# Kernel optimization log

Hardware: AMD Instinct MI355X
Metric: run time of the kernel (lower is better)

Reference implementation:

```python
import jax, jax.numpy as jnp
import numpy as np

N_NODES = 100000
N_EDGES = 1600000
IN_F = 256
OUT_F = 128


def setup_inputs() -> dict:
    key = jax.random.key(0)
    k1, k2, k3, k4, k5, k6 = jax.random.split(key, 6)
    x = jax.random.normal(k1, (N_NODES, IN_F), dtype=jnp.float32)
    edge_row = jax.random.randint(k2, (N_EDGES,), 0, N_NODES, dtype=jnp.int32)
    edge_col = jax.random.randint(k3, (N_EDGES,), 0, N_NODES, dtype=jnp.int32)
    edge_val = jax.random.uniform(k4, (N_EDGES,), dtype=jnp.float32)
    # xavier_uniform for W: bound = sqrt(6/(fan_in+fan_out))
    bound_w = float(np.sqrt(6.0 / (IN_F + OUT_F)))
    W = jax.random.uniform(k5, (IN_F, OUT_F), dtype=jnp.float32, minval=-bound_w, maxval=bound_w)
    stdv = 1.0 / float(np.sqrt(OUT_F))
    b = jax.random.uniform(k6, (OUT_F,), dtype=jnp.float32, minval=-stdv, maxval=stdv)
    return {"x": x, "edge_row": edge_row, "edge_col": edge_col, "edge_val": edge_val, "W": W, "b": b}


def reference(x, edge_row, edge_col, edge_val, W, b):
    # dropout p=0.0 -> identity
    support = x @ W + b                      # [N, out]
    # sparse adjacency matmul: out[r] += val * support[c] over edges (r, c, val)
    msgs = edge_val[:, None] * support[edge_col]          # [E, out]
    out = jax.ops.segment_sum(msgs, edge_row, num_segments=N_NODES)  # [N, out]
    return jax.nn.relu(out)
```

## Files before the change

kernel.cpp:

```cpp
#include <hip/hip_runtime.h>


constexpr int kNodes = 100000;
constexpr int kEdges = 1600000;
constexpr int kInF   = 256;
constexpr int kOutF  = 128;
constexpr int kTiles = kNodes / 16;
constexpr int kScanBlocks = (kNodes + 255) / 256;
constexpr int kBucketBlocks = 800;
constexpr int kGemmBlocks = 1250;

constexpr int kNB = 256;
constexpr int kRB = 391;
constexpr int kCap = 7808;

typedef __attribute__((ext_vector_type(8))) short short8;
typedef __attribute__((ext_vector_type(8))) unsigned short ush8;
typedef __attribute__((ext_vector_type(4))) float floatx4;

__device__ inline unsigned short f2bf_rne(float f) {
    unsigned int u = __float_as_uint(f);
    unsigned int r = u + 0x7FFFu + ((u >> 16) & 1u);
    return (unsigned short)(r >> 16);
}
__device__ inline float bf2f(unsigned short h) {
    return __uint_as_float(((unsigned int)h) << 16);
}

__device__ inline short8 cvt8_bf16(const float4 a, const float4 b) {
    union { short8 s; unsigned int u[4]; } r;
    asm("v_cvt_pk_bf16_f32 %0, %1, %2" : "=v"(r.u[0]) : "v"(a.x), "v"(a.y));
    asm("v_cvt_pk_bf16_f32 %0, %1, %2" : "=v"(r.u[1]) : "v"(a.z), "v"(a.w));
    asm("v_cvt_pk_bf16_f32 %0, %1, %2" : "=v"(r.u[2]) : "v"(b.x), "v"(b.y));
    asm("v_cvt_pk_bf16_f32 %0, %1, %2" : "=v"(r.u[3]) : "v"(b.z), "v"(b.w));
    return r.s;
}

__device__ inline void gload_lds16(const void* g, void* l) {
    __builtin_amdgcn_global_load_lds(
        (const __attribute__((address_space(1))) unsigned int*)g,
        (__attribute__((address_space(3))) unsigned int*)l,
        16, 0, 0);
}

__global__ __launch_bounds__(256) void gcn_gemm(const float* __restrict__ x,
                                                const float* __restrict__ W,
                                                const float* __restrict__ b,
                                                unsigned short* __restrict__ support) {
    __shared__ __align__(16) float lbuf[2][4096];

    const int lane = threadIdx.x & 63;
    const int wv   = threadIdx.x >> 6;
    const int rowl = lane & 15;
    const int quad = lane >> 4;
    const int colbase = wv * 32;

    short8 bfrag[2][8];
#pragma unroll
    for (int ct = 0; ct < 2; ++ct) {
        const int col = colbase + ct * 16 + rowl;
#pragma unroll
        for (int kc = 0; kc < 8; ++kc) {
            const int kb = kc * 32 + quad * 8;
            short8 f;
#pragma unroll
            for (int j = 0; j < 8; ++j)
                f[j] = (short)f2bf_rne(W[(size_t)(kb + j) * kOutF + col]);
            bfrag[ct][kc] = f;
        }
    }
    const float bias0 = b[colbase + rowl];
    const float bias1 = b[colbase + 16 + rowl];

    const int G = gridDim.x;
    int t = blockIdx.x;

#define GEMM_STAGE(buf_, tile_)                                                   \
    do {                                                                          \
        const float* tb_ = x + (size_t)(tile_) * 16 * kInF;                       \
        _Pragma("unroll")                                                         \
        for (int i_ = 0; i_ < 4; ++i_) {                                          \
            const int row_ = i_ * 4 + wv;                                         \
            gload_lds16(tb_ + (size_t)row_ * kInF + ((lane ^ (row_ & 7)) << 2),   \
                        &lbuf[buf_][row_ << 8]);                                  \
        }                                                                         \
    } while (0)

    if (t < kTiles) GEMM_STAGE(0, t);
    int cur = 0;

    for (; t < kTiles; t += G) {
        const int tn = t + G;
        asm volatile("s_waitcnt vmcnt(0)" ::: "memory");
        __syncthreads();
        if (tn < kTiles) GEMM_STAGE(cur ^ 1, tn);

        const int r0 = t * 16;
        const float* base = &lbuf[cur][rowl << 8];
        const int rsw = rowl & 7;
        floatx4 acc0 = {0.f, 0.f, 0.f, 0.f};
        floatx4 acc1 = {0.f, 0.f, 0.f, 0.f};
#pragma unroll
        for (int kc = 0; kc < 8; ++kc) {
            const int g0 = (kc << 3) + (quad << 1);
            const float4 v0 = *reinterpret_cast<const float4*>(base + ((g0 ^ rsw) << 2));
            const float4 v1 = *reinterpret_cast<const float4*>(base + (((g0 + 1) ^ rsw) << 2));
            const short8 a = cvt8_bf16(v0, v1);
            acc0 = __builtin_amdgcn_mfma_f32_16x16x32_bf16(a, bfrag[0][kc], acc0, 0, 0, 0);
            acc1 = __builtin_amdgcn_mfma_f32_16x16x32_bf16(a, bfrag[1][kc], acc1, 0, 0, 0);
        }
#pragma unroll
        for (int reg = 0; reg < 4; ++reg) {
            const size_t rbase = (size_t)(r0 + quad * 4 + reg) * kOutF + colbase;
            support[rbase + rowl]      = f2bf_rne(acc0[reg] + bias0);
            support[rbase + 16 + rowl] = f2bf_rne(acc1[reg] + bias1);
        }
        cur ^= 1;
    }
#undef GEMM_STAGE
}

__global__ __launch_bounds__(256) void gcn_hist(const int* __restrict__ erow,
                                                int* __restrict__ counts) {
    const int stride = gridDim.x * blockDim.x;
    for (int e = blockIdx.x * blockDim.x + threadIdx.x; e < kEdges; e += stride)
        atomicAdd(&counts[erow[e]], 1);
}

__global__ __launch_bounds__(256) void gcn_scan1(const int* __restrict__ counts,
                                                 int* __restrict__ row_start,
                                                 int* __restrict__ blockSums) {
    __shared__ int s[256];
    const int i = blockIdx.x * 256 + threadIdx.x;
    const int v = (i < kNodes) ? counts[i] : 0;
    s[threadIdx.x] = v;
    __syncthreads();
#pragma unroll
    for (int off = 1; off < 256; off <<= 1) {
        const int t = (threadIdx.x >= off) ? s[threadIdx.x - off] : 0;
        __syncthreads();
        s[threadIdx.x] += t;
        __syncthreads();
    }
    if (i < kNodes) row_start[i] = s[threadIdx.x] - v;
    if (threadIdx.x == 255) blockSums[blockIdx.x] = s[255];
}

__global__ __launch_bounds__(512) void gcn_scan2(const int* __restrict__ blockSums,
                                                 int* __restrict__ blockOffs) {
    __shared__ int s[512];
    const int v = (threadIdx.x < kScanBlocks) ? blockSums[threadIdx.x] : 0;
    s[threadIdx.x] = v;
    __syncthreads();
#pragma unroll
    for (int off = 1; off < 512; off <<= 1) {
        const int t = (threadIdx.x >= off) ? s[threadIdx.x - off] : 0;
        __syncthreads();
        s[threadIdx.x] += t;
        __syncthreads();
    }
    if (threadIdx.x < kScanBlocks) blockOffs[threadIdx.x] = s[threadIdx.x] - v;
}

__global__ __launch_bounds__(256) void gcn_scan3(int* __restrict__ row_start,
                                                 const int* __restrict__ blockOffs,
                                                 int* __restrict__ cursor,
                                                 int* __restrict__ bucket_cursor) {
    const int i = blockIdx.x * 256 + threadIdx.x;
    if (i < kNodes) {
        const int rs = row_start[i] + blockOffs[blockIdx.x];
        row_start[i] = rs;
        cursor[i]    = rs;
        if (i % kRB == 0) bucket_cursor[i / kRB] = rs;
    }
    if (i == 0) row_start[kNodes] = kEdges;
}

__global__ __launch_bounds__(256) void gcn_bin(const int* __restrict__ erow,
                                               const int* __restrict__ ecol,
                                               const float* __restrict__ eval,
                                               int* __restrict__ bucket_cursor,
                                               int2* __restrict__ packed) {
    __shared__ int cnt[kNB];
    __shared__ int base[kNB];
    __shared__ int rk[kNB];
    const int T   = kBucketBlocks * 256;
    const int tid = blockIdx.x * 256 + threadIdx.x;

    cnt[threadIdx.x] = 0;
    rk[threadIdx.x]  = 0;

    int bk[8], pk[8], vb[8];
    bool ok[8];
#pragma unroll
    for (int i = 0; i < 8; ++i) {
        const int e = tid + i * T;
        ok[i] = (e < kEdges);
        const int r = ok[i] ? erow[e] : 0;
        const int c = ok[i] ? ecol[e] : 0;
        const float v = ok[i] ? eval[e] : 0.f;
        const unsigned int b = (unsigned int)r / (unsigned int)kRB;
        bk[i] = (int)b;
        pk[i] = ((r - (int)b * kRB) << 17) | c;
        vb[i] = __float_as_int(v);
    }
    __syncthreads();
#pragma unroll
    for (int i = 0; i < 8; ++i)
        if (ok[i]) atomicAdd(&cnt[bk[i]], 1);
    __syncthreads();
    const int c = cnt[threadIdx.x];
    base[threadIdx.x] = c ? atomicAdd(&bucket_cursor[threadIdx.x], c) : 0;
    __syncthreads();
#pragma unroll
    for (int i = 0; i < 8; ++i) {
        if (ok[i]) {
            const int r = atomicAdd(&rk[bk[i]], 1);
            packed[base[bk[i]] + r] = make_int2(pk[i], vb[i]);
        }
    }
}

__global__ __launch_bounds__(256) void gcn_place(const int* __restrict__ row_start,
                                                 int* __restrict__ cursor,
                                                 int2* __restrict__ packed) {
    __shared__ int2 st[kCap];
    const int bk = blockIdx.x;
    const int r0 = bk * kRB;
    const int r1 = min(r0 + kRB, kNodes);
    if (r0 >= kNodes) return;
    const int s0 = row_start[r0];
    const int s1 = row_start[r1];
    const int size   = s1 - s0;
    const int staged = min(size, kCap);

    for (int i = threadIdx.x; i < staged; i += 256)
        st[i] = packed[s0 + i];

    int2 tail[8];
    int  nt = 0;
    for (int i = kCap + threadIdx.x; i < size; i += 256)
        if (nt < 8) tail[nt++] = packed[s0 + i];

    __syncthreads();

    for (int i = threadIdx.x; i < staged; i += 256) {
        const int2 p  = st[i];
        const int row = r0 + (p.x >> 17);
        const int pos = atomicAdd(&cursor[row], 1);
        packed[pos] = make_int2(p.x & 0x1FFFF, p.y);
    }
#pragma unroll
    for (int t = 0; t < 8; ++t) {
        if (t < nt) {
            const int2 p  = tail[t];
            const int row = r0 + (p.x >> 17);
            const int pos = atomicAdd(&cursor[row], 1);
            packed[pos] = make_int2(p.x & 0x1FFFF, p.y);
        }
    }
}

__global__ __launch_bounds__(256) void gcn_aggregate(const int* __restrict__ row_start,
                                                     const int2* __restrict__ packed,
                                                     const unsigned short* __restrict__ support,
                                                     float* __restrict__ out) {
    const int n  = blockIdx.x * 16 + (threadIdx.x >> 4);
    const int f8 = (threadIdx.x & 15) * 8;
    if (n >= kNodes) return;
    const int s0 = row_start[n];
    const int s1 = row_start[n + 1];
    float acc[8];
#pragma unroll
    for (int j = 0; j < 8; ++j) acc[j] = 0.f;

    int i = s0;
    for (; i + 3 < s1; i += 4) {
        const int2 p0 = packed[i];
        const int2 p1 = packed[i + 1];
        const int2 p2 = packed[i + 2];
        const int2 p3 = packed[i + 3];
        const ush8 a0 = *reinterpret_cast<const ush8*>(support + (size_t)p0.x * kOutF + f8);
        const ush8 a1 = *reinterpret_cast<const ush8*>(support + (size_t)p1.x * kOutF + f8);
        const ush8 a2 = *reinterpret_cast<const ush8*>(support + (size_t)p2.x * kOutF + f8);
        const ush8 a3 = *reinterpret_cast<const ush8*>(support + (size_t)p3.x * kOutF + f8);
        const float v0 = __int_as_float(p0.y), v1 = __int_as_float(p1.y);
        const float v2 = __int_as_float(p2.y), v3 = __int_as_float(p3.y);
#pragma unroll
        for (int j = 0; j < 8; ++j) {
            acc[j] += v0 * bf2f(a0[j]);
            acc[j] += v1 * bf2f(a1[j]);
            acc[j] += v2 * bf2f(a2[j]);
            acc[j] += v3 * bf2f(a3[j]);
        }
    }
    for (; i < s1; ++i) {
        const int2 p = packed[i];
        const float v = __int_as_float(p.y);
        const ush8 a = *reinterpret_cast<const ush8*>(support + (size_t)p.x * kOutF + f8);
#pragma unroll
        for (int j = 0; j < 8; ++j) acc[j] += v * bf2f(a[j]);
    }

    float4 o0 = make_float4(fmaxf(acc[0], 0.f), fmaxf(acc[1], 0.f),
                            fmaxf(acc[2], 0.f), fmaxf(acc[3], 0.f));
    float4 o1 = make_float4(fmaxf(acc[4], 0.f), fmaxf(acc[5], 0.f),
                            fmaxf(acc[6], 0.f), fmaxf(acc[7], 0.f));
    *reinterpret_cast<float4*>(out + (size_t)n * kOutF + f8)     = o0;
    *reinterpret_cast<float4*>(out + (size_t)n * kOutF + f8 + 4) = o1;
}

extern "C" void kernel_launch(void* const* d_in, const int* in_sizes, int n_in,
                              void* d_out, int out_size, void* d_ws, size_t ws_size,
                              hipStream_t stream) {
    const float* x    = (const float*)d_in[0];
    const int*   erow = (const int*)  d_in[1];
    const int*   ecol = (const int*)  d_in[2];
    const float* eval = (const float*)d_in[3];
    const float* W    = (const float*)d_in[4];
    const float* b    = (const float*)d_in[5];
    float* out = (float*)d_out;

    char* ws = (char*)d_ws;
    unsigned short* support = (unsigned short*)(ws);
    int2* packed    = (int2*)(ws + 25600000);
    int*  counts    = (int*) (ws + 38400000);
    int*  row_start = (int*) (ws + 38800000);
    int*  cursor    = (int*) (ws + 39200008);
    int*  blockSums = (int*) (ws + 39600008);
    int*  blockOffs = (int*) (ws + 39601576);
    int*  bucket_cursor = counts;

    gcn_gemm<<<kGemmBlocks, 256, 0, stream>>>(x, W, b, support);

    hipMemsetAsync(counts, 0, (size_t)kNodes * sizeof(int), stream);
    gcn_hist  <<<1024, 256, 0, stream>>>(erow, counts);
    gcn_scan1 <<<kScanBlocks, 256, 0, stream>>>(counts, row_start, blockSums);
    gcn_scan2 <<<1, 512, 0, stream>>>(blockSums, blockOffs);
    gcn_scan3 <<<kScanBlocks, 256, 0, stream>>>(row_start, blockOffs, cursor, bucket_cursor);
    gcn_bin   <<<kBucketBlocks, 256, 0, stream>>>(erow, ecol, eval, bucket_cursor, packed);
    gcn_place <<<kNB, 256, 0, stream>>>(row_start, cursor, packed);

    gcn_aggregate<<<(kNodes + 15) / 16, 256, 0, stream>>>(row_start, packed, support, out);
}
```

Baseline: 398.7 us.

## Replace per-row histogram and three-pass scan with bucket histogram and in-block row scan

```diff
diff --git a/kernel.cpp b/kernel.cpp
--- a/kernel.cpp
+++ b/kernel.cpp
@@ -6,13 +6,12 @@
 constexpr int kInF   = 256;
 constexpr int kOutF  = 128;
 constexpr int kTiles = kNodes / 16;
-constexpr int kScanBlocks = (kNodes + 255) / 256;
 constexpr int kBucketBlocks = 800;
 constexpr int kGemmBlocks = 1250;
 
 constexpr int kNB = 256;
 constexpr int kRB = 391;
-constexpr int kCap = 7808;
+constexpr int kCap = 7424;
 
 typedef __attribute__((ext_vector_type(8))) short short8;
 typedef __attribute__((ext_vector_type(8))) unsigned short ush8;
@@ -120,19 +119,25 @@
 #undef GEMM_STAGE
 }
 
-__global__ __launch_bounds__(256) void gcn_hist(const int* __restrict__ erow,
-                                                int* __restrict__ counts) {
+__global__ __launch_bounds__(256) void gcn_bhist(const int* __restrict__ erow,
+                                                 int* __restrict__ bucket_tot) {
+    __shared__ int cnt[kNB];
+    cnt[threadIdx.x] = 0;
+    __syncthreads();
     const int stride = gridDim.x * blockDim.x;
     for (int e = blockIdx.x * blockDim.x + threadIdx.x; e < kEdges; e += stride)
-        atomicAdd(&counts[erow[e]], 1);
-}
-
-__global__ __launch_bounds__(256) void gcn_scan1(const int* __restrict__ counts,
-                                                 int* __restrict__ row_start,
-                                                 int* __restrict__ blockSums) {
+        atomicAdd(&cnt[(unsigned int)erow[e] / (unsigned int)kRB], 1);
+    __syncthreads();
+    const int c = cnt[threadIdx.x];
+    if (c) atomicAdd(&bucket_tot[threadIdx.x], c);
+}
+
+__global__ __launch_bounds__(256) void gcn_bscan(const int* __restrict__ bucket_tot,
+                                                 int* __restrict__ bucket_base,
+                                                 int* __restrict__ bucket_cursor,
+                                                 int* __restrict__ row_start) {
     __shared__ int s[256];
-    const int i = blockIdx.x * 256 + threadIdx.x;
-    const int v = (i < kNodes) ? counts[i] : 0;
+    const int v = bucket_tot[threadIdx.x];
     s[threadIdx.x] = v;
     __syncthreads();
 #pragma unroll
@@ -142,38 +147,13 @@
         s[threadIdx.x] += t;
         __syncthreads();
     }
-    if (i < kNodes) row_start[i] = s[threadIdx.x] - v;
-    if (threadIdx.x == 255) blockSums[blockIdx.x] = s[255];
-}
-
-__global__ __launch_bounds__(512) void gcn_scan2(const int* __restrict__ blockSums,
-                                                 int* __restrict__ blockOffs) {
-    __shared__ int s[512];
-    const int v = (threadIdx.x < kScanBlocks) ? blockSums[threadIdx.x] : 0;
-    s[threadIdx.x] = v;
-    __syncthreads();
-#pragma unroll
-    for (int off = 1; off < 512; off <<= 1) {
-        const int t = (threadIdx.x >= off) ? s[threadIdx.x - off] : 0;
-        __syncthreads();
-        s[threadIdx.x] += t;
-        __syncthreads();
-    }
-    if (threadIdx.x < kScanBlocks) blockOffs[threadIdx.x] = s[threadIdx.x] - v;
-}
-
-__global__ __launch_bounds__(256) void gcn_scan3(int* __restrict__ row_start,
-                                                 const int* __restrict__ blockOffs,
-                                                 int* __restrict__ cursor,
-                                                 int* __restrict__ bucket_cursor) {
-    const int i = blockIdx.x * 256 + threadIdx.x;
-    if (i < kNodes) {
-        const int rs = row_start[i] + blockOffs[blockIdx.x];
-        row_start[i] = rs;
-        cursor[i]    = rs;
-        if (i % kRB == 0) bucket_cursor[i / kRB] = rs;
-    }
-    if (i == 0) row_start[kNodes] = kEdges;
+    const int excl = s[threadIdx.x] - v;
+    bucket_base[threadIdx.x]   = excl;
+    bucket_cursor[threadIdx.x] = excl;
+    if (threadIdx.x == 255) {
+        bucket_base[256]   = kEdges;
+        row_start[kNodes]  = kEdges;
+    }
 }
 
 __global__ __launch_bounds__(256) void gcn_bin(const int* __restrict__ erow,
@@ -221,41 +201,71 @@
     }
 }
 
-__global__ __launch_bounds__(256) void gcn_place(const int* __restrict__ row_start,
-                                                 int* __restrict__ cursor,
+__global__ __launch_bounds__(256) void gcn_place(const int* __restrict__ bucket_base,
+                                                 int* __restrict__ row_start,
                                                  int2* __restrict__ packed) {
     __shared__ int2 st[kCap];
+    __shared__ int  s[512];
+    __shared__ int  rcur[kRB + 1];
     const int bk = blockIdx.x;
     const int r0 = bk * kRB;
     const int r1 = min(r0 + kRB, kNodes);
-    if (r0 >= kNodes) return;
-    const int s0 = row_start[r0];
-    const int s1 = row_start[r1];
-    const int size   = s1 - s0;
+    const int NR = r1 - r0;
+    if (NR <= 0) return;
+    const int bb = bucket_base[bk];
+    const int s1 = bucket_base[bk + 1];
+    const int size   = s1 - bb;
     const int staged = min(size, kCap);
-
-    for (int i = threadIdx.x; i < staged; i += 256)
-        st[i] = packed[s0 + i];
-
+    const int tid = threadIdx.x;
+
+    s[tid] = 0;
+    s[tid + 256] = 0;
+    __syncthreads();
+
+    for (int i = tid; i < staged; i += 256) {
+        const int2 p = packed[bb + i];
+        st[i] = p;
+        atomicAdd(&s[p.x >> 17], 1);
+    }
     int2 tail[8];
     int  nt = 0;
-    for (int i = kCap + threadIdx.x; i < size; i += 256)
-        if (nt < 8) tail[nt++] = packed[s0 + i];
-
-    __syncthreads();
-
-    for (int i = threadIdx.x; i < staged; i += 256) {
+    for (int i = kCap + tid; i < size; i += 256) {
+        if (nt < 8) {
+            tail[nt] = packed[bb + i];
+            atomicAdd(&s[tail[nt].x >> 17], 1);
+            ++nt;
+        }
+    }
+    __syncthreads();
+
+    const int i0 = tid, i1 = tid + 256;
+#pragma unroll
+    for (int off = 1; off < 512; off <<= 1) {
+        const int v0 = (i0 >= off) ? s[i0 - off] : 0;
+        const int v1 = (i1 >= off) ? s[i1 - off] : 0;
+        __syncthreads();
+        s[i0] += v0;
+        s[i1] += v1;
+        __syncthreads();
+    }
+
+    for (int i = tid; i < NR; i += 256) {
+        const int excl = i ? s[i - 1] : 0;
+        row_start[r0 + i] = bb + excl;
+        rcur[i] = excl;
+    }
+    __syncthreads();
+
+    for (int i = tid; i < staged; i += 256) {
         const int2 p  = st[i];
-        const int row = r0 + (p.x >> 17);
-        const int pos = atomicAdd(&cursor[row], 1);
+        const int pos = bb + atomicAdd(&rcur[p.x >> 17], 1);
         packed[pos] = make_int2(p.x & 0x1FFFF, p.y);
     }
 #pragma unroll
     for (int t = 0; t < 8; ++t) {
         if (t < nt) {
             const int2 p  = tail[t];
-            const int row = r0 + (p.x >> 17);
-            const int pos = atomicAdd(&cursor[row], 1);
+            const int pos = bb + atomicAdd(&rcur[p.x >> 17], 1);
             packed[pos] = make_int2(p.x & 0x1FFFF, p.y);
         }
     }
@@ -323,23 +333,19 @@
 
     char* ws = (char*)d_ws;
     unsigned short* support = (unsigned short*)(ws);
-    int2* packed    = (int2*)(ws + 25600000);
-    int*  counts    = (int*) (ws + 38400000);
-    int*  row_start = (int*) (ws + 38800000);
-    int*  cursor    = (int*) (ws + 39200008);
-    int*  blockSums = (int*) (ws + 39600008);
-    int*  blockOffs = (int*) (ws + 39601576);
-    int*  bucket_cursor = counts;
+    int2* packed        = (int2*)(ws + 25600000);
+    int*  row_start     = (int*) (ws + 38400000);
+    int*  bucket_tot    = (int*) (ws + 38800008);
+    int*  bucket_base   = (int*) (ws + 38801032);
+    int*  bucket_cursor = (int*) (ws + 38802060);
 
     gcn_gemm<<<kGemmBlocks, 256, 0, stream>>>(x, W, b, support);
 
-    hipMemsetAsync(counts, 0, (size_t)kNodes * sizeof(int), stream);
-    gcn_hist  <<<1024, 256, 0, stream>>>(erow, counts);
-    gcn_scan1 <<<kScanBlocks, 256, 0, stream>>>(counts, row_start, blockSums);
-    gcn_scan2 <<<1, 512, 0, stream>>>(blockSums, blockOffs);
-    gcn_scan3 <<<kScanBlocks, 256, 0, stream>>>(row_start, blockOffs, cursor, bucket_cursor);
-    gcn_bin   <<<kBucketBlocks, 256, 0, stream>>>(erow, ecol, eval, bucket_cursor, packed);
-    gcn_place <<<kNB, 256, 0, stream>>>(row_start, cursor, packed);
+    hipMemsetAsync(bucket_tot, 0, kNB * sizeof(int), stream);
+    gcn_bhist<<<1024, 256, 0, stream>>>(erow, bucket_tot);
+    gcn_bscan<<<1, 256, 0, stream>>>(bucket_tot, bucket_base, bucket_cursor, row_start);
+    gcn_bin  <<<kBucketBlocks, 256, 0, stream>>>(erow, ecol, eval, bucket_cursor, packed);
+    gcn_place<<<kNB, 256, 0, stream>>>(bucket_base, row_start, packed);
 
     gcn_aggregate<<<(kNodes + 15) / 16, 256, 0, stream>>>(row_start, packed, support, out);
 }
```

After: 358.5 us. -10.1%, faster.
